# Optimization experiments

Measured on AMD Instinct MI355X. Metric: run time of the kernel, lower is better.

Reference implementation:

```python
import jax, jax.numpy as jnp
import numpy as np

EPS = 1e-6


def setup_inputs() -> dict:
    key = jax.random.key(0)
    ks = jax.random.split(key, 7)
    T, B, D, N = 512, 32, 1024, 128
    scale_w = (6.0 / (N + D)) ** 0.5  # xavier_uniform bound
    def w(k):
        return jax.random.uniform(k, (N, D), jnp.float32, -scale_w, scale_w)
    return {
        "x": jax.random.normal(ks[0], (T, B, D), jnp.float32),
        "S0": jnp.zeros((B, N, N), jnp.float32),
        "W_k": w(ks[1]),
        "W_v": w(ks[2]),
        "W_q": w(ks[3]),
        "W_erase": w(ks[4]),
        "W_write": w(ks[5]),
    }


def _ntm_forward(x, S0, W_k, W_v, W_q, W_erase, W_write):
    # Projections for all timesteps at once: (T, B, n_state)
    k = jnp.einsum('tbd,nd->tbn', x, W_k)
    v = jnp.einsum('tbd,nd->tbn', x, W_v)
    q = jnp.einsum('tbd,nd->tbn', x, W_q)
    erase = jnp.einsum('tbd,nd->tbn', x, W_erase)  # use_sigmoid=False: raw
    write = jnp.einsum('tbd,nd->tbn', x, W_write)

    def step(S, inp):
        k_t, v_t, q_t, e_t, w_t = inp
        k_norm = k_t / (jnp.linalg.norm(k_t, axis=-1, keepdims=True) + EPS)
        # S: (B, n, n); outer products via broadcasting
        erase_outer = e_t[:, :, None] * k_norm[:, None, :]
        write_outer = (w_t * v_t)[:, :, None] * k_norm[:, None, :]
        S_new = jnp.tanh(S * (1.0 - erase_outer) + write_outer)
        Sq = jnp.einsum('bij,bj->bi', S_new, q_t)
        out = Sq * jax.nn.silu(Sq)
        return S_new, out

    S_final, outputs = jax.lax.scan(step, S0, (k, v, q, erase, write))
    return outputs, S_final


def reference(x, S0, W_k, W_v, W_q, W_erase, W_write):
    return _ntm_forward(x, S0, W_k, W_v, W_q, W_erase, W_write)
```

## Files before the change

kernel.cpp:

```cpp
#include <hip/hip_runtime.h>
#include <hip/hip_bf16.h>


typedef __attribute__((ext_vector_type(8))) short bf16x8;
typedef __attribute__((ext_vector_type(4))) float f32x4;
typedef __attribute__((ext_vector_type(2))) float f32x2;
typedef __attribute__((ext_vector_type(4))) unsigned short u16x4;

static constexpr int T_STEPS = 512;
static constexpr int BATCH   = 32;
static constexpr int DDIM    = 1024;
static constexpr int NDIM    = 128;
static constexpr int LDC     = 5 * NDIM;
static constexpr int MROWS   = T_STEPS * BATCH;
static constexpr int OUT_N   = T_STEPS * BATCH * NDIM;

__device__ __forceinline__ void split2(float v, unsigned short& hi, unsigned short& lo) {
    unsigned u  = __builtin_bit_cast(unsigned, v);
    unsigned uh = u & 0xFFFF0000u;
    hi = (unsigned short)(uh >> 16);
    float d = v - __builtin_bit_cast(float, uh);
    lo = (unsigned short)(__builtin_bit_cast(unsigned, d) >> 16);
}

static constexpr int LSTR = 40;
static constexpr int OAH = 0, OAL = 128 * LSTR, OBH = 2 * 128 * LSTR, OBL = 3 * 128 * LSTR;

__global__ __launch_bounds__(256, 3) void gemm_kernel(
    const float* __restrict__ x,
    const float* __restrict__ w0, const float* __restrict__ w1,
    const float* __restrict__ w2, const float* __restrict__ w3,
    const float* __restrict__ w4,
    float* __restrict__ C)
{
    __shared__ unsigned short lds[4 * 128 * LSTR];

    const float* Ws[5] = {w0, w1, w2, w3, w4};
    const int id  = blockIdx.x;
    const int xcd = id & 7;
    const int kq  = id >> 3;
    const int bn  = kq % 5;
    const int bm  = (kq / 5) * 8 + xcd;

    const int tid  = threadIdx.x;
    const int wave = tid >> 6, lane = tid & 63;
    const int quad = lane >> 4, l16 = lane & 15;
    const int wm = (wave >> 1) * 64, wn = (wave & 1) * 64;
    const int m0 = bm * 128;
    const float* wsrc = Ws[bn];

    f32x4 acc[4][4];
#pragma unroll
    for (int i = 0; i < 4; ++i)
#pragma unroll
        for (int j = 0; j < 4; ++j) acc[i][j] = (f32x4)(0.0f);

    const int srow = tid >> 3;
    const int sc4  = tid & 7;
    const int fa = (wm + l16) * LSTR + quad * 8;
    const int fb = (wn + l16) * LSTR + quad * 8;

    const float* xp[4];
    const float* wp[4];
#pragma unroll
    for (int i = 0; i < 4; ++i) {
        xp[i] = x    + (size_t)(m0 + srow + i * 32) * DDIM + sc4 * 4;
        wp[i] = wsrc + (size_t)(srow + i * 32) * DDIM + sc4 * 4;
    }

    f32x4 ra[4], rb[4];
#pragma unroll
    for (int i = 0; i < 4; ++i) { ra[i] = *(const f32x4*)xp[i]; rb[i] = *(const f32x4*)wp[i]; }

    for (int kk = 0; kk < 32; ++kk) {
#pragma unroll
        for (int i = 0; i < 4; ++i) {
            u16x4 ha, la, hb, lb;
#pragma unroll
            for (int j = 0; j < 4; ++j) {
                unsigned short h, l;
                split2(ra[i][j], h, l); ha[j] = h; la[j] = l;
                split2(rb[i][j], h, l); hb[j] = h; lb[j] = l;
            }
            const int o = (srow + i * 32) * LSTR + sc4 * 4;
            *(u16x4*)&lds[OAH + o] = ha;
            *(u16x4*)&lds[OAL + o] = la;
            *(u16x4*)&lds[OBH + o] = hb;
            *(u16x4*)&lds[OBL + o] = lb;
        }
        __syncthreads();

        const int kn = (kk + 1 < 32) ? kk + 1 : 31;
#pragma unroll
        for (int i = 0; i < 4; ++i) {
            ra[i] = *(const f32x4*)(xp[i] + kn * 32);
            rb[i] = *(const f32x4*)(wp[i] + kn * 32);
        }

        bf16x8 ah[4], bh[4];
#pragma unroll
        for (int i = 0; i < 4; ++i) {
            ah[i] = *(const bf16x8*)&lds[OAH + fa + i * 16 * LSTR];
            bh[i] = *(const bf16x8*)&lds[OBH + fb + i * 16 * LSTR];
        }
#pragma unroll
        for (int mi = 0; mi < 4; ++mi)
#pragma unroll
            for (int ni = 0; ni < 4; ++ni)
                acc[mi][ni] = __builtin_amdgcn_mfma_f32_16x16x32_bf16(
                    ah[mi], bh[ni], acc[mi][ni], 0, 0, 0);
        {
            bf16x8 bl[4];
#pragma unroll
            for (int i = 0; i < 4; ++i)
                bl[i] = *(const bf16x8*)&lds[OBL + fb + i * 16 * LSTR];
#pragma unroll
            for (int mi = 0; mi < 4; ++mi)
#pragma unroll
                for (int ni = 0; ni < 4; ++ni)
                    acc[mi][ni] = __builtin_amdgcn_mfma_f32_16x16x32_bf16(
                        ah[mi], bl[ni], acc[mi][ni], 0, 0, 0);
        }
        {
            bf16x8 al[4];
#pragma unroll
            for (int i = 0; i < 4; ++i)
                al[i] = *(const bf16x8*)&lds[OAL + fa + i * 16 * LSTR];
#pragma unroll
            for (int mi = 0; mi < 4; ++mi)
#pragma unroll
                for (int ni = 0; ni < 4; ++ni)
                    acc[mi][ni] = __builtin_amdgcn_mfma_f32_16x16x32_bf16(
                        al[mi], bh[ni], acc[mi][ni], 0, 0, 0);
        }
        __syncthreads();
    }

#pragma unroll
    for (int mi = 0; mi < 4; ++mi)
#pragma unroll
        for (int ni = 0; ni < 4; ++ni) {
            const int row = m0 + wm + mi * 16 + quad * 4;
            const int col = bn * 128 + wn + ni * 16 + l16;
#pragma unroll
            for (int r = 0; r < 4; ++r)
                C[(size_t)(row + r) * LDC + col] = acc[mi][ni][r];
        }
}

__global__ __launch_bounds__(256) void knorm_kernel(float* __restrict__ C)
{
    const int r    = blockIdx.x * 4 + (threadIdx.x >> 6);
    const int lane = threadIdx.x & 63;
    float* base = C + (size_t)r * LDC;

    f32x2 k2 = *(const f32x2*)(base + lane * 2);
    f32x2 v2 = *(const f32x2*)(base + NDIM + lane * 2);
    f32x2 w2 = *(const f32x2*)(base + 4 * NDIM + lane * 2);

    float ss = k2.x * k2.x + k2.y * k2.y;
#pragma unroll
    for (int off = 32; off >= 1; off >>= 1) ss += __shfl_xor(ss, off, 64);
    float inv = __builtin_amdgcn_rcpf(sqrtf(ss) + 1e-6f);

    f32x2 kn = {k2.x * inv, k2.y * inv};
    f32x2 wv = {v2.x * w2.x, v2.y * w2.y};
    *(f32x2*)(base + lane * 2) = kn;
    *(f32x2*)(base + NDIM + lane * 2) = wv;
}

__device__ __forceinline__ float tanh_fast(float xx) {
    float ex = __builtin_amdgcn_exp2f(xx * 2.8853900817779268f);
    float r  = __builtin_amdgcn_rcpf(ex + 1.0f);
    return fmaf(-2.0f, r, 1.0f);
}

template <int CTRL, int RMASK>
__device__ __forceinline__ float dpp_add(float x) {
    int yi = __builtin_amdgcn_update_dpp(
        0, __builtin_bit_cast(int, x), CTRL, RMASK, 0xF, true);
    return x + __builtin_bit_cast(float, yi);
}

__device__ __forceinline__ float dpp_reduce32(float x) {
    x = dpp_add<0xB1,  0xF>(x);
    x = dpp_add<0x4E,  0xF>(x);
    x = dpp_add<0x141, 0xF>(x);
    x = dpp_add<0x140, 0xF>(x);
    x = dpp_add<0x142, 0xA>(x);
    return x;
}

__global__ __launch_bounds__(256) void ntm_scan_kernel(
    const float* __restrict__ C, const float* __restrict__ S0,
    float* __restrict__ out)
{
    const int L    = blockIdx.x;
    const int b    = (L & 7) + 8 * ((L >> 3) & 3);
    const int row  = (L >> 5) * 8 + (threadIdx.x >> 5);
    const int g    = threadIdx.x & 31;
    const int col0 = g * 4;

    f32x4 S = *(const f32x4*)(S0 + ((size_t)b * NDIM + row) * NDIM + col0);

    const size_t STRIDE = (size_t)BATCH * LDC;
    const float* pb = C + (size_t)b * LDC;

    f32x4 kS[4], qS[4];
    float eS[4], wvS[4];

#pragma unroll
    for (int s = 0; s < 2; ++s) {
        const float* p = pb + (size_t)s * STRIDE;
        kS[s]  = *(const f32x4*)(p + col0);
        qS[s]  = *(const f32x4*)(p + 2 * NDIM + col0);
        eS[s]  = p[3 * NDIM + row];
        wvS[s] = p[NDIM + row];
    }

    float* op = out + (size_t)b * NDIM + row;

    for (int ti = 0; ti < T_STEPS / 4; ++ti) {
#pragma unroll
        for (int j = 0; j < 4; ++j) {
            const int t = ti * 4 + j;
            {
                int tp = t + 2;
                if (tp > T_STEPS - 1) tp = T_STEPS - 1;
                const float* p = pb + (size_t)tp * STRIDE;
                const int ps = (j + 2) & 3;
                kS[ps]  = *(const f32x4*)(p + col0);
                qS[ps]  = *(const f32x4*)(p + 2 * NDIM + col0);
                eS[ps]  = p[3 * NDIM + row];
                wvS[ps] = p[NDIM + row];
            }
            float dot = 0.0f;
#pragma unroll
            for (int u = 0; u < 4; ++u) {
                float t0  = fmaf(-eS[j], S[u], wvS[j]);
                float pre = fmaf(kS[j][u], t0, S[u]);
                S[u] = tanh_fast(pre);
                dot = fmaf(S[u], qS[j][u], dot);
            }
            dot = dpp_reduce32(dot);

            if ((threadIdx.x & 31) == 31)
                op[(size_t)t * BATCH * NDIM] = dot;
        }
    }

    *(f32x4*)(out + (size_t)T_STEPS * BATCH * NDIM
              + ((size_t)b * NDIM + row) * NDIM + col0) = S;
}

__global__ __launch_bounds__(256) void silu_kernel(float* __restrict__ out)
{
    const int i = blockIdx.x * 256 + threadIdx.x;
    f32x4 d = ((const f32x4*)out)[i];
    f32x4 y;
#pragma unroll
    for (int j = 0; j < 4; ++j) {
        float sg = __builtin_amdgcn_rcpf(
            1.0f + __builtin_amdgcn_exp2f(-d[j] * 1.4426950408889634f));
        y[j] = d[j] * d[j] * sg;
    }
    ((f32x4*)out)[i] = y;
}

extern "C" void kernel_launch(void* const* d_in, const int* in_sizes, int n_in,
                              void* d_out, int out_size, void* d_ws, size_t ws_size,
                              hipStream_t stream) {
    const float* x  = (const float*)d_in[0];
    const float* S0 = (const float*)d_in[1];
    const float* wk = (const float*)d_in[2];
    const float* wv = (const float*)d_in[3];
    const float* wq = (const float*)d_in[4];
    const float* we = (const float*)d_in[5];
    const float* ww = (const float*)d_in[6];
    float* out = (float*)d_out;
    float* C   = (float*)d_ws;

    gemm_kernel<<<640, 256, 0, stream>>>(x, wk, wv, wq, we, ww, C);
    knorm_kernel<<<MROWS / 4, 256, 0, stream>>>(C);
    ntm_scan_kernel<<<512, 256, 0, stream>>>(C, S0, out);
    silu_kernel<<<OUT_N / 1024, 256, 0, stream>>>(out);
}
```

Measured before the change: 291.8 us.

## Pre-split inputs into bf16 hi/lo planes before the projection GEMM

```diff
diff --git a/kernel.cpp b/kernel.cpp
--- a/kernel.cpp
+++ b/kernel.cpp
@@ -6,6 +6,7 @@
 typedef __attribute__((ext_vector_type(4))) float f32x4;
 typedef __attribute__((ext_vector_type(2))) float f32x2;
 typedef __attribute__((ext_vector_type(4))) unsigned short u16x4;
+typedef __attribute__((ext_vector_type(8))) unsigned short u16x8;
 
 static constexpr int T_STEPS = 512;
 static constexpr int BATCH   = 32;
@@ -15,6 +16,11 @@
 static constexpr int MROWS   = T_STEPS * BATCH;
 static constexpr int OUT_N   = T_STEPS * BATCH * NDIM;
 
+static constexpr size_t C_BYTES    = (size_t)MROWS * LDC * 4;
+static constexpr size_t XS_ELEMS   = (size_t)MROWS * DDIM;
+static constexpr size_t WSP_ELEMS  = 5ull * NDIM * DDIM;
+static constexpr size_t NEED_BYTES = C_BYTES + 4 * XS_ELEMS + 4 * WSP_ELEMS;
+
 __device__ __forceinline__ void split2(float v, unsigned short& hi, unsigned short& lo) {
     unsigned u  = __builtin_bit_cast(unsigned, v);
     unsigned uh = u & 0xFFFF0000u;
@@ -23,8 +29,176 @@
     lo = (unsigned short)(__builtin_bit_cast(unsigned, d) >> 16);
 }
 
+__global__ __launch_bounds__(256) void split_kernel(
+    const float* __restrict__ x,
+    const float* __restrict__ w0, const float* __restrict__ w1,
+    const float* __restrict__ w2, const float* __restrict__ w3,
+    const float* __restrict__ w4,
+    unsigned short* __restrict__ xhi, unsigned short* __restrict__ xlo,
+    unsigned short* __restrict__ whi, unsigned short* __restrict__ wlo)
+{
+    const size_t idx = (size_t)blockIdx.x * 256 + threadIdx.x;
+    const size_t e = idx * 4;
+
+    const float* src;
+    unsigned short* dh;
+    unsigned short* dl;
+    if (e < XS_ELEMS) {
+        src = x + e;
+        dh = xhi + e;
+        dl = xlo + e;
+    } else {
+        const size_t wi = e - XS_ELEMS;
+        const int n = (int)(wi >> 17);
+        const size_t off = wi & 131071;
+        const float* wp = w0;
+        if (n == 1) wp = w1;
+        else if (n == 2) wp = w2;
+        else if (n == 3) wp = w3;
+        else if (n == 4) wp = w4;
+        src = wp + off;
+        dh = whi + wi;
+        dl = wlo + wi;
+    }
+
+    f32x4 v = *(const f32x4*)src;
+    u16x4 h, l;
+#pragma unroll
+    for (int j = 0; j < 4; ++j) {
+        unsigned short hh, ll;
+        split2(v[j], hh, ll);
+        h[j] = hh; l[j] = ll;
+    }
+    *(u16x4*)dh = h;
+    *(u16x4*)dl = l;
+}
+
 static constexpr int LSTR = 40;
 static constexpr int OAH = 0, OAL = 128 * LSTR, OBH = 2 * 128 * LSTR, OBL = 3 * 128 * LSTR;
+
+__global__ __launch_bounds__(256, 3) void gemm2_kernel(
+    const unsigned short* __restrict__ xhi, const unsigned short* __restrict__ xlo,
+    const unsigned short* __restrict__ whi, const unsigned short* __restrict__ wlo,
+    float* __restrict__ C)
+{
+    __shared__ unsigned short lds[4 * 128 * LSTR];
+
+    const int id  = blockIdx.x;
+    const int xcd = id & 7;
+    const int kq  = id >> 3;
+    const int bn  = kq % 5;
+    const int bm  = (kq / 5) * 8 + xcd;
+
+    const int tid  = threadIdx.x;
+    const int wave = tid >> 6, lane = tid & 63;
+    const int quad = lane >> 4, l16 = lane & 15;
+    const int wm = (wave >> 1) * 64, wn = (wave & 1) * 64;
+    const int m0 = bm * 128;
+
+    f32x4 acc[4][4];
+#pragma unroll
+    for (int i = 0; i < 4; ++i)
+#pragma unroll
+        for (int j = 0; j < 4; ++j) acc[i][j] = (f32x4)(0.0f);
+
+    const int srow4 = tid >> 2;
+    const int sc8   = (tid & 3) * 8;
+    const int fa = (wm + l16) * LSTR + quad * 8;
+    const int fb = (wn + l16) * LSTR + quad * 8;
+
+    const unsigned short* pah[2];
+    const unsigned short* pal[2];
+    const unsigned short* pbh[2];
+    const unsigned short* pbl[2];
+#pragma unroll
+    for (int i = 0; i < 2; ++i) {
+        const size_t xoff = (size_t)(m0 + srow4 + i * 64) * DDIM + sc8;
+        const size_t woff = (size_t)bn * (NDIM * DDIM) + (size_t)(srow4 + i * 64) * DDIM + sc8;
+        pah[i] = xhi + xoff;
+        pal[i] = xlo + xoff;
+        pbh[i] = whi + woff;
+        pbl[i] = wlo + woff;
+    }
+
+    u16x8 rah[2], ral[2], rbh[2], rbl[2];
+#pragma unroll
+    for (int i = 0; i < 2; ++i) {
+        rah[i] = *(const u16x8*)pah[i];
+        ral[i] = *(const u16x8*)pal[i];
+        rbh[i] = *(const u16x8*)pbh[i];
+        rbl[i] = *(const u16x8*)pbl[i];
+    }
+
+    for (int kk = 0; kk < 32; ++kk) {
+#pragma unroll
+        for (int i = 0; i < 2; ++i) {
+            const int o = (srow4 + i * 64) * LSTR + sc8;
+            *(u16x8*)&lds[OAH + o] = rah[i];
+            *(u16x8*)&lds[OAL + o] = ral[i];
+            *(u16x8*)&lds[OBH + o] = rbh[i];
+            *(u16x8*)&lds[OBL + o] = rbl[i];
+        }
+        __syncthreads();
+
+        const int kn = ((kk + 1 < 32) ? kk + 1 : 31) * 32;
+#pragma unroll
+        for (int i = 0; i < 2; ++i) {
+            rah[i] = *(const u16x8*)(pah[i] + kn);
+            ral[i] = *(const u16x8*)(pal[i] + kn);
+            rbh[i] = *(const u16x8*)(pbh[i] + kn);
+            rbl[i] = *(const u16x8*)(pbl[i] + kn);
+        }
+
+        bf16x8 ah[4], bh[4];
+#pragma unroll
+        for (int i = 0; i < 4; ++i) {
+            ah[i] = *(const bf16x8*)&lds[OAH + fa + i * 16 * LSTR];
+            bh[i] = *(const bf16x8*)&lds[OBH + fb + i * 16 * LSTR];
+        }
+#pragma unroll
+        for (int mi = 0; mi < 4; ++mi)
+#pragma unroll
+            for (int ni = 0; ni < 4; ++ni)
+                acc[mi][ni] = __builtin_amdgcn_mfma_f32_16x16x32_bf16(
+                    ah[mi], bh[ni], acc[mi][ni], 0, 0, 0);
+        {
+            bf16x8 bl[4];
+#pragma unroll
+            for (int i = 0; i < 4; ++i)
+                bl[i] = *(const bf16x8*)&lds[OBL + fb + i * 16 * LSTR];
+#pragma unroll
+            for (int mi = 0; mi < 4; ++mi)
+#pragma unroll
+                for (int ni = 0; ni < 4; ++ni)
+                    acc[mi][ni] = __builtin_amdgcn_mfma_f32_16x16x32_bf16(
+                        ah[mi], bl[ni], acc[mi][ni], 0, 0, 0);
+        }
+        {
+            bf16x8 al[4];
+#pragma unroll
+            for (int i = 0; i < 4; ++i)
+                al[i] = *(const bf16x8*)&lds[OAL + fa + i * 16 * LSTR];
+#pragma unroll
+            for (int mi = 0; mi < 4; ++mi)
+#pragma unroll
+                for (int ni = 0; ni < 4; ++ni)
+                    acc[mi][ni] = __builtin_amdgcn_mfma_f32_16x16x32_bf16(
+                        al[mi], bh[ni], acc[mi][ni], 0, 0, 0);
+        }
+        __syncthreads();
+    }
+
+#pragma unroll
+    for (int mi = 0; mi < 4; ++mi)
+#pragma unroll
+        for (int ni = 0; ni < 4; ++ni) {
+            const int row = m0 + wm + mi * 16 + quad * 4;
+            const int col = bn * 128 + wn + ni * 16 + l16;
+#pragma unroll
+            for (int r = 0; r < 4; ++r)
+                C[(size_t)(row + r) * LDC + col] = acc[mi][ni][r];
+        }
+}
 
 __global__ __launch_bounds__(256, 3) void gemm_kernel(
     const float* __restrict__ x,
@@ -280,7 +454,17 @@
     float* out = (float*)d_out;
     float* C   = (float*)d_ws;
 
-    gemm_kernel<<<640, 256, 0, stream>>>(x, wk, wv, wq, we, ww, C);
+    if (ws_size >= NEED_BYTES) {
+        unsigned short* xhi = (unsigned short*)((char*)d_ws + C_BYTES);
+        unsigned short* xlo = xhi + XS_ELEMS;
+        unsigned short* whi = xlo + XS_ELEMS;
+        unsigned short* wlo = whi + WSP_ELEMS;
+        const int nblk = (int)((XS_ELEMS / 4 + WSP_ELEMS / 4) / 256);
+        split_kernel<<<nblk, 256, 0, stream>>>(x, wk, wv, wq, we, ww, xhi, xlo, whi, wlo);
+        gemm2_kernel<<<640, 256, 0, stream>>>(xhi, xlo, whi, wlo, C);
+    } else {
+        gemm_kernel<<<640, 256, 0, stream>>>(x, wk, wv, wq, we, ww, C);
+    }
     knorm_kernel<<<MROWS / 4, 256, 0, stream>>>(C);
     ntm_scan_kernel<<<512, 256, 0, stream>>>(C, S0, out);
     silu_kernel<<<OUT_N / 1024, 256, 0, stream>>>(out);
```

Measured after the change: 310.2 us. 6.3% more time.

## Use single-pass bf16 GEMM and deepen scan prefetch to four steps

Applied to the files above, without the earlier changes.

```diff
diff --git a/kernel.cpp b/kernel.cpp
--- a/kernel.cpp
+++ b/kernel.cpp
@@ -15,25 +15,23 @@
 static constexpr int MROWS   = T_STEPS * BATCH;
 static constexpr int OUT_N   = T_STEPS * BATCH * NDIM;
 
-__device__ __forceinline__ void split2(float v, unsigned short& hi, unsigned short& lo) {
-    unsigned u  = __builtin_bit_cast(unsigned, v);
-    unsigned uh = u & 0xFFFF0000u;
-    hi = (unsigned short)(uh >> 16);
-    float d = v - __builtin_bit_cast(float, uh);
-    lo = (unsigned short)(__builtin_bit_cast(unsigned, d) >> 16);
+__device__ __forceinline__ unsigned short rne_bf16(float v) {
+    unsigned u = __builtin_bit_cast(unsigned, v);
+    u += 0x7FFFu + ((u >> 16) & 1u);
+    return (unsigned short)(u >> 16);
 }
 
 static constexpr int LSTR = 40;
-static constexpr int OAH = 0, OAL = 128 * LSTR, OBH = 2 * 128 * LSTR, OBL = 3 * 128 * LSTR;
-
-__global__ __launch_bounds__(256, 3) void gemm_kernel(
+static constexpr int OA = 0, OB = 128 * LSTR;
+
+__global__ __launch_bounds__(256, 3) void gemm3_kernel(
     const float* __restrict__ x,
     const float* __restrict__ w0, const float* __restrict__ w1,
     const float* __restrict__ w2, const float* __restrict__ w3,
     const float* __restrict__ w4,
     float* __restrict__ C)
 {
-    __shared__ unsigned short lds[4 * 128 * LSTR];
+    __shared__ unsigned short lds[2 * 128 * LSTR];
 
     const float* Ws[5] = {w0, w1, w2, w3, w4};
     const int id  = blockIdx.x;
@@ -75,18 +73,15 @@
     for (int kk = 0; kk < 32; ++kk) {
 #pragma unroll
         for (int i = 0; i < 4; ++i) {
-            u16x4 ha, la, hb, lb;
+            u16x4 ha, hb;
 #pragma unroll
             for (int j = 0; j < 4; ++j) {
-                unsigned short h, l;
-                split2(ra[i][j], h, l); ha[j] = h; la[j] = l;
-                split2(rb[i][j], h, l); hb[j] = h; lb[j] = l;
+                ha[j] = rne_bf16(ra[i][j]);
+                hb[j] = rne_bf16(rb[i][j]);
             }
             const int o = (srow + i * 32) * LSTR + sc4 * 4;
-            *(u16x4*)&lds[OAH + o] = ha;
-            *(u16x4*)&lds[OAL + o] = la;
-            *(u16x4*)&lds[OBH + o] = hb;
-            *(u16x4*)&lds[OBL + o] = lb;
+            *(u16x4*)&lds[OA + o] = ha;
+            *(u16x4*)&lds[OB + o] = hb;
         }
         __syncthreads();
 
@@ -100,8 +95,8 @@
         bf16x8 ah[4], bh[4];
 #pragma unroll
         for (int i = 0; i < 4; ++i) {
-            ah[i] = *(const bf16x8*)&lds[OAH + fa + i * 16 * LSTR];
-            bh[i] = *(const bf16x8*)&lds[OBH + fb + i * 16 * LSTR];
+            ah[i] = *(const bf16x8*)&lds[OA + fa + i * 16 * LSTR];
+            bh[i] = *(const bf16x8*)&lds[OB + fb + i * 16 * LSTR];
         }
 #pragma unroll
         for (int mi = 0; mi < 4; ++mi)
@@ -109,30 +104,6 @@
             for (int ni = 0; ni < 4; ++ni)
                 acc[mi][ni] = __builtin_amdgcn_mfma_f32_16x16x32_bf16(
                     ah[mi], bh[ni], acc[mi][ni], 0, 0, 0);
-        {
-            bf16x8 bl[4];
-#pragma unroll
-            for (int i = 0; i < 4; ++i)
-                bl[i] = *(const bf16x8*)&lds[OBL + fb + i * 16 * LSTR];
-#pragma unroll
-            for (int mi = 0; mi < 4; ++mi)
-#pragma unroll
-                for (int ni = 0; ni < 4; ++ni)
-                    acc[mi][ni] = __builtin_amdgcn_mfma_f32_16x16x32_bf16(
-                        ah[mi], bl[ni], acc[mi][ni], 0, 0, 0);
-        }
-        {
-            bf16x8 al[4];
-#pragma unroll
-            for (int i = 0; i < 4; ++i)
-                al[i] = *(const bf16x8*)&lds[OAL + fa + i * 16 * LSTR];
-#pragma unroll
-            for (int mi = 0; mi < 4; ++mi)
-#pragma unroll
-                for (int ni = 0; ni < 4; ++ni)
-                    acc[mi][ni] = __builtin_amdgcn_mfma_f32_16x16x32_bf16(
-                        al[mi], bh[ni], acc[mi][ni], 0, 0, 0);
-        }
         __syncthreads();
     }
 
@@ -206,11 +177,11 @@
     const size_t STRIDE = (size_t)BATCH * LDC;
     const float* pb = C + (size_t)b * LDC;
 
-    f32x4 kS[4], qS[4];
-    float eS[4], wvS[4];
-
-#pragma unroll
-    for (int s = 0; s < 2; ++s) {
+    f32x4 kS[8], qS[8];
+    float eS[8], wvS[8];
+
+#pragma unroll
+    for (int s = 0; s < 4; ++s) {
         const float* p = pb + (size_t)s * STRIDE;
         kS[s]  = *(const f32x4*)(p + col0);
         qS[s]  = *(const f32x4*)(p + 2 * NDIM + col0);
@@ -220,15 +191,15 @@
 
     float* op = out + (size_t)b * NDIM + row;
 
-    for (int ti = 0; ti < T_STEPS / 4; ++ti) {
-#pragma unroll
-        for (int j = 0; j < 4; ++j) {
-            const int t = ti * 4 + j;
+    for (int ti = 0; ti < T_STEPS / 8; ++ti) {
+#pragma unroll
+        for (int j = 0; j < 8; ++j) {
+            const int t = ti * 8 + j;
             {
-                int tp = t + 2;
+                int tp = t + 4;
                 if (tp > T_STEPS - 1) tp = T_STEPS - 1;
                 const float* p = pb + (size_t)tp * STRIDE;
-                const int ps = (j + 2) & 3;
+                const int ps = (j + 4) & 7;
                 kS[ps]  = *(const f32x4*)(p + col0);
                 qS[ps]  = *(const f32x4*)(p + 2 * NDIM + col0);
                 eS[ps]  = p[3 * NDIM + row];
@@ -280,7 +251,7 @@
     float* out = (float*)d_out;
     float* C   = (float*)d_ws;
 
-    gemm_kernel<<<640, 256, 0, stream>>>(x, wk, wv, wq, we, ww, C);
+    gemm3_kernel<<<640, 256, 0, stream>>>(x, wk, wv, wq, we, ww, C);
     knorm_kernel<<<MROWS / 4, 256, 0, stream>>>(C);
     ntm_scan_kernel<<<512, 256, 0, stream>>>(C, S0, out);
     silu_kernel<<<OUT_N / 1024, 256, 0, stream>>>(out);
```

New measurement: 276.3 us. 5.3% less time.
